# Kernel tuning notes

Hardware: AMD Instinct MI355X
Metric: run time of the kernel (lower is better)

The kernel has to match this reference:

```python
import jax, jax.numpy as jnp
import numpy as np

B, S, DIN, D, H, NL, DOUT = 1, 1024, 128, 512, 8, 4, 390
HD = D // H
MAXS = 1024  # max_seq_length; Er has 2*MAXS-1 rows
EPS = 1e-5


def _ln(x, g, b):
    m = jnp.mean(x, axis=-1, keepdims=True)
    v = jnp.mean((x - m) ** 2, axis=-1, keepdims=True)
    return (x - m) / jnp.sqrt(v + EPS) * g + b


def setup_inputs() -> dict:
    key = jax.random.key(0)
    ks = jax.random.split(key, 16)
    it = iter(ks)

    def w(shape, scale=0.02):
        return jax.random.normal(next(it), shape, jnp.float32) * scale

    return {
        "x": jax.random.normal(next(it), (B, S, DIN), jnp.float32),
        "emb_W": w((DIN, D)), "emb_b": jnp.zeros((D,), jnp.float32),
        "Wq": w((NL, D, D)), "bq": jnp.zeros((NL, D), jnp.float32),
        "Wk": w((NL, D, D)), "bk": jnp.zeros((NL, D), jnp.float32),
        "Wv": w((NL, D, D)), "bv": jnp.zeros((NL, D), jnp.float32),
        "Wo": w((NL, D, D)), "bo": jnp.zeros((NL, D), jnp.float32),
        "Er": w((NL, 2 * MAXS - 1, HD), 1.0),  # torch.randn init
        "ln1_g": jnp.ones((NL, D), jnp.float32), "ln1_b": jnp.zeros((NL, D), jnp.float32),
        "W1": w((NL, D, 4 * D)), "b1": jnp.zeros((NL, 4 * D), jnp.float32),
        "W2": w((NL, 4 * D, D)), "b2": jnp.zeros((NL, D), jnp.float32),
        "ln2_g": jnp.ones((NL, D), jnp.float32), "ln2_b": jnp.zeros((NL, D), jnp.float32),
        "lnf_g": jnp.ones((D,), jnp.float32), "lnf_b": jnp.zeros((D,), jnp.float32),
        "Wi": w((D, 2 * D)), "bi": jnp.zeros((2 * D,), jnp.float32),
        "Wf": w((2 * D, DOUT)), "bf": jnp.zeros((DOUT,), jnp.float32),
    }


def reference(x, emb_W, emb_b, Wq, bq, Wk, bk, Wv, bv, Wo, bo, Er,
              ln1_g, ln1_b, W1, b1, W2, b2, ln2_g, ln2_b,
              lnf_g, lnf_b, Wi, bi, Wf, bf):
    h = x @ emb_W + emb_b  # (B,S,D)
    # relative index table (S,S): (i - j) + S - 1, shared by all layers
    ri = (jnp.arange(S)[:, None] - jnp.arange(S)[None, :]) + (S - 1)
    scale = 1.0 / jnp.sqrt(jnp.float32(HD))
    for l in range(NL):
        res = h
        n = _ln(h, ln1_g[l], ln1_b[l])
        q = (n @ Wq[l] + bq[l]).reshape(B, S, H, HD).transpose(0, 2, 1, 3)  # (B,H,S,HD)
        k = (n @ Wk[l] + bk[l]).reshape(B, S, H, HD).transpose(0, 2, 1, 3)
        v = (n @ Wv[l] + bv[l]).reshape(B, S, H, HD).transpose(0, 2, 1, 3)
        scores = jnp.einsum('bhsd,bhtd->bhst', q, k) * scale  # (B,H,S,S)
        E = Er[l][ri]  # (S,S,HD) gathered relative embeddings
        rel = jnp.einsum('bhsd,std->bhst', q, E)  # note: NOT scaled (faithful)
        attn = jax.nn.softmax(scores + rel, axis=-1)  # no causal mask in source
        o = jnp.einsum('bhst,bhtd->bhsd', attn, v)
        o = o.transpose(0, 2, 1, 3).reshape(B, S, D)
        h = res + (o @ Wo[l] + bo[l])
        res = h
        n = _ln(h, ln2_g[l], ln2_b[l])
        f = jax.nn.gelu(n @ W1[l] + b1[l], approximate=False) @ W2[l] + b2[l]
        h = res + f
    h = _ln(h, lnf_g, lnf_b)
    h = jax.nn.gelu(h @ Wi + bi, approximate=False)
    return h @ Wf + bf  # (B,S,DOUT)
```

## Files before the change

### kernel.cpp

```cpp
#include <hip/hip_runtime.h>
#include <hip/hip_bf16.h>
#include <math.h>

#define SEQ 1024
#define DM 512
#define NH 8
#define HD 64
#define NLAYER 4
#define DIN 128
#define DFF 2048
#define DOUT 390
#define ERROWS 2047
#define NSPLIT 4

using u16 = unsigned short;
typedef __attribute__((ext_vector_type(8))) short short8;
typedef __attribute__((ext_vector_type(4))) float f32x4;

__device__ inline u16 f2bf(float f){
  __hip_bfloat16 h = __float2bfloat16(f);
  return *(u16*)&h;
}
__device__ inline float bf2f(u16 u){
  __hip_bfloat16 h; *(u16*)&h = u;
  return __bfloat162float(h);
}

__device__ inline float block_sum(float v, float* red){
  int tid = threadIdx.x;
  red[tid] = v; __syncthreads();
  for (int s = 128; s > 0; s >>= 1){
    if (tid < s) red[tid] += red[tid + s];
    __syncthreads();
  }
  float r = red[0]; __syncthreads();
  return r;
}

__global__ __launch_bounds__(256)
void prep_k(const float* __restrict__ x, const float* __restrict__ Er,
            const float* __restrict__ bq, const float* __restrict__ bk,
            const float* __restrict__ bv,
            const float* __restrict__ emb_W, const float* __restrict__ Wq,
            const float* __restrict__ Wk, const float* __restrict__ Wv,
            const float* __restrict__ Wo, const float* __restrict__ W1,
            const float* __restrict__ W2, const float* __restrict__ Wi,
            const float* __restrict__ Wf,
            u16* __restrict__ xb, u16* __restrict__ erB,
            float* __restrict__ qkvbias,
            u16* __restrict__ embT, u16* __restrict__ wqkvT,
            u16* __restrict__ woT, u16* __restrict__ w1T,
            u16* __restrict__ w2T, u16* __restrict__ wiT,
            u16* __restrict__ wfT)
{
  __shared__ float Ls[64][65];
  int b = blockIdx.x;
  const int tid = threadIdx.x;

  if (b < 128){
    int i = (b * 256 + tid) * 4;
    float4 v = *(const float4*)(x + i);
    xb[i+0]=f2bf(v.x); xb[i+1]=f2bf(v.y); xb[i+2]=f2bf(v.z); xb[i+3]=f2bf(v.w);
    return;
  }
  b -= 128;
  if (b < 512){
    int i = (b * 256 + tid) * 4;
    if (i < NLAYER * ERROWS * HD){
      float4 v = *(const float4*)(Er + i);
      erB[i+0]=f2bf(v.x); erB[i+1]=f2bf(v.y); erB[i+2]=f2bf(v.z); erB[i+3]=f2bf(v.w);
    }
    return;
  }
  b -= 512;
  if (b < 24){
    int i = b * 256 + tid;
    int l = i / 1536, c = i - l * 1536;
    float v = (c < 512) ? bq[l * 512 + c]
            : (c < 1024) ? bk[l * 512 + c - 512]
                         : bv[l * 512 + c - 1024];
    qkvbias[i] = v;
    return;
  }
  b -= 24;

  const float* W; u16* WT; int K, N, k0, n0;
  if (b < 16){
    W = emb_W; WT = embT; K = DIN; N = DM;
    k0 = (b & 1) * 64; n0 = (b >> 1) * 64;
  } else if (b < 1040){
    int i = b - 16, fam = i >> 8, w2 = i & 255, z = w2 >> 6, t2 = w2 & 63;
    K = DM; N = DM; k0 = (t2 & 7) * 64; n0 = (t2 >> 3) * 64;
    const float* Wsrc = (fam == 0) ? Wq : (fam == 1) ? Wk : (fam == 2) ? Wv : Wo;
    W = Wsrc + (long)z * DM * DM;
    WT = (fam < 3) ? wqkvT + (long)z * 1536 * DM + (long)fam * 512 * DM
                   : woT + (long)z * DM * DM;
  } else if (b < 2064){
    int i = b - 1040, z = i >> 8, w2 = i & 255;
    K = DM; N = DFF; k0 = (w2 & 7) * 64; n0 = (w2 >> 3) * 64;
    W = W1 + (long)z * DM * DFF; WT = w1T + (long)z * DFF * DM;
  } else if (b < 3088){
    int i = b - 2064, z = i >> 8, w2 = i & 255;
    K = DFF; N = DM; k0 = (w2 & 31) * 64; n0 = (w2 >> 5) * 64;
    W = W2 + (long)z * DFF * DM; WT = w2T + (long)z * DM * DFF;
  } else if (b < 3216){
    int i = b - 3088;
    K = DM; N = 2 * DM; k0 = (i & 7) * 64; n0 = (i >> 3) * 64;
    W = Wi; WT = wiT;
  } else {
    int i = b - 3216;
    K = 2 * DM; N = DOUT; k0 = (i & 15) * 64; n0 = (i >> 4) * 64;
    W = Wf; WT = wfT;
  }

  const int cr = (tid & 15) * 4, rr0 = tid >> 4;
#pragma unroll
  for (int rr = 0; rr < 4; rr++){
    int row = rr0 + rr * 16;
    const float* wp = W + (size_t)(k0 + row) * N + n0 + cr;
#pragma unroll
    for (int j = 0; j < 4; j++)
      Ls[row][cr + j] = (n0 + cr + j < N) ? wp[j] : 0.f;
  }
  __syncthreads();
  const int nrow = tid >> 2, kc = (tid & 3) * 16;
  const bool valid = (n0 + nrow) < N;
  u16 buf[16];
#pragma unroll
  for (int j = 0; j < 16; j++)
    buf[j] = valid ? f2bf(Ls[kc + j][nrow]) : (u16)0;
  u16* out = WT + (size_t)(n0 + nrow) * K + k0 + kc;
  ((uint4*)out)[0] = ((uint4*)buf)[0];
  ((uint4*)out)[1] = ((uint4*)buf)[1];
}

template<bool GELU, bool RES, bool BIAS, bool OUTBF>
__global__ __launch_bounds__(256)
void mgemm(const u16* __restrict__ A, const u16* __restrict__ B,
           const float* __restrict__ bias, const float* __restrict__ res,
           void* __restrict__ Cout, int N, int K,
           int lda, int ldb, int ldc)
{
  __shared__ u16 As[32][72];
  __shared__ u16 Bs[64][72];
  const int tid = threadIdx.x;
  const int row0 = blockIdx.y * 32, n0 = blockIdx.x * 64;
  const int w = tid >> 6, lane = tid & 63, m = lane & 15, quad = lane >> 4;
  const int rowg = w >> 1, colp = w & 1;
  const int ar = tid >> 3, akc = (tid & 7) * 8;
  const int br = tid >> 2, bkc = (tid & 3) * 16;

  f32x4 acc[2];
  acc[0] = (f32x4){0.f,0.f,0.f,0.f};
  acc[1] = (f32x4){0.f,0.f,0.f,0.f};

  uint4 pa  = *(const uint4*)&A[(long)(row0 + ar) * lda + akc];
  uint4 pb0 = *(const uint4*)&B[(long)(n0 + br) * ldb + bkc];
  uint4 pb1 = *(const uint4*)&B[(long)(n0 + br) * ldb + bkc + 8];

  for (int k0 = 0; k0 < K; k0 += 64){
    *(uint4*)&As[ar][akc]     = pa;
    *(uint4*)&Bs[br][bkc]     = pb0;
    *(uint4*)&Bs[br][bkc + 8] = pb1;
    __syncthreads();
    if (k0 + 64 < K){
      pa  = *(const uint4*)&A[(long)(row0 + ar) * lda + k0 + 64 + akc];
      pb0 = *(const uint4*)&B[(long)(n0 + br) * ldb + k0 + 64 + bkc];
      pb1 = *(const uint4*)&B[(long)(n0 + br) * ldb + k0 + 64 + bkc + 8];
    }
    short8 a0 = *(const short8*)&As[rowg * 16 + m][quad * 8];
    short8 a1 = *(const short8*)&As[rowg * 16 + m][32 + quad * 8];
#pragma unroll
    for (int c = 0; c < 2; c++){
      int colg = colp * 2 + c;
      short8 b0 = *(const short8*)&Bs[colg * 16 + m][quad * 8];
      short8 b1 = *(const short8*)&Bs[colg * 16 + m][32 + quad * 8];
      acc[c] = __builtin_amdgcn_mfma_f32_16x16x32_bf16(a0, b0, acc[c], 0, 0, 0);
      acc[c] = __builtin_amdgcn_mfma_f32_16x16x32_bf16(a1, b1, acc[c], 0, 0, 0);
    }
    __syncthreads();
  }

#pragma unroll
  for (int c = 0; c < 2; c++){
    int col = n0 + (colp * 2 + c) * 16 + m;
    if (col < N){
#pragma unroll
      for (int r = 0; r < 4; r++){
        int row = row0 + rowg * 16 + quad * 4 + r;
        float val = acc[c][r];
        if (BIAS) val += bias[col];
        if (RES)  val += res[(long)row * ldc + col];
        if (GELU) val = 0.5f * val * (1.f + erff(val * 0.70710678118f));
        if (OUTBF) ((u16*)Cout)[(long)row * ldc + col] = f2bf(val);
        else      ((float*)Cout)[(long)row * ldc + col] = val;
      }
    }
  }
}

__global__ __launch_bounds__(256)
void ln_k(const float* __restrict__ x, const float* __restrict__ g,
          const float* __restrict__ b, u16* __restrict__ out)
{
  __shared__ float red[256];
  const int r = blockIdx.x, tid = threadIdx.x;
  const float* xr = x + (size_t)r * DM;
  float v0 = xr[tid], v1 = xr[tid + 256];
  float mean = block_sum(v0 + v1, red) * (1.f / DM);
  float d0 = v0 - mean, d1 = v1 - mean;
  float var = block_sum(d0 * d0 + d1 * d1, red) * (1.f / DM);
  float inv = rsqrtf(var + 1e-5f);
  out[(size_t)r * DM + tid]       = f2bf(d0 * inv * g[tid]       + b[tid]);
  out[(size_t)r * DM + tid + 256] = f2bf(d1 * inv * g[tid + 256] + b[tid + 256]);
}

__global__ __launch_bounds__(256)
void flash_k(const u16* __restrict__ qkv, const u16* __restrict__ ErB,
             float* __restrict__ Op, float* __restrict__ ml)
{
  __shared__ u16 Qs[64][72];
  __shared__ u16 Ks[64][72];
  __shared__ u16 VsT[64][72];
  __shared__ u16 Es[128][72];
  __shared__ u16 Ts[64][136];
  __shared__ u16 Ps[64][72];

  const int tid = threadIdx.x;
  const int s0 = blockIdx.x * 64, hh = blockIdx.y, sp = blockIdx.z;
  const int w = tid >> 6, lane = tid & 63, m = lane & 15, quad = lane >> 4;

  {
    const int r = tid >> 2, kc = (tid & 3) * 16;
    const u16* qp = qkv + (size_t)(s0 + r) * 1536 + hh * HD + kc;
    *(uint4*)&Qs[r][kc]     = *(const uint4*)&qp[0];
    *(uint4*)&Qs[r][kc + 8] = *(const uint4*)&qp[8];
  }
  __syncthreads();

  const short8 a0 = *(const short8*)&Qs[w * 16 + m][quad * 8];
  const short8 a1 = *(const short8*)&Qs[w * 16 + m][32 + quad * 8];

  f32x4 accO[4];
#pragma unroll
  for (int c = 0; c < 4; c++) accO[c] = (f32x4){0.f, 0.f, 0.f, 0.f};
  float mrun[4], lrun[4];
#pragma unroll
  for (int r = 0; r < 4; r++){ mrun[r] = -1e30f; lrun[r] = 0.f; }

  const int tbeg = sp * (SEQ / NSPLIT), tend = tbeg + SEQ / NSPLIT;
  for (int t0 = tbeg; t0 < tend; t0 += 64){
    __syncthreads();
    {
      const int r = tid >> 2, kc = (tid & 3) * 16;
      const u16* kp = qkv + (size_t)(t0 + r) * 1536 + 512 + hh * HD + kc;
      *(uint4*)&Ks[r][kc]     = *(const uint4*)&kp[0];
      *(uint4*)&Ks[r][kc + 8] = *(const uint4*)&kp[8];
      const u16* vp = qkv + (size_t)(t0 + r) * 1536 + 1024 + hh * HD + kc;
      uint4 v0 = *(const uint4*)&vp[0];
      uint4 v1 = *(const uint4*)&vp[8];
      const u16* pv0 = (const u16*)&v0;
      const u16* pv1 = (const u16*)&v1;
#pragma unroll
      for (int j = 0; j < 8; j++) VsT[kc + j][r]     = pv0[j];
#pragma unroll
      for (int j = 0; j < 8; j++) VsT[kc + 8 + j][r] = pv1[j];
      const int rb = s0 - t0 + 960;
      for (int idx = tid; idx < 127 * 8; idx += 256){
        int er = idx >> 3, ekc = (idx & 7) * 8;
        *(uint4*)&Es[er][ekc] = *(const uint4*)&ErB[(size_t)(rb + er) * HD + ekc];
      }
      if (tid < 8){ uint4 z = {0,0,0,0}; *(uint4*)&Es[127][tid * 8] = z; }
    }
    __syncthreads();

    f32x4 qk[4], tt[8];
#pragma unroll
    for (int c = 0; c < 4; c++) qk[c] = (f32x4){0.f,0.f,0.f,0.f};
#pragma unroll
    for (int c = 0; c < 8; c++) tt[c] = (f32x4){0.f,0.f,0.f,0.f};
#pragma unroll
    for (int c = 0; c < 4; c++){
      short8 b0 = *(const short8*)&Ks[c * 16 + m][quad * 8];
      short8 b1 = *(const short8*)&Ks[c * 16 + m][32 + quad * 8];
      qk[c] = __builtin_amdgcn_mfma_f32_16x16x32_bf16(a0, b0, qk[c], 0, 0, 0);
      qk[c] = __builtin_amdgcn_mfma_f32_16x16x32_bf16(a1, b1, qk[c], 0, 0, 0);
    }
#pragma unroll
    for (int c = 0; c < 8; c++){
      short8 b0 = *(const short8*)&Es[c * 16 + m][quad * 8];
      short8 b1 = *(const short8*)&Es[c * 16 + m][32 + quad * 8];
      tt[c] = __builtin_amdgcn_mfma_f32_16x16x32_bf16(a0, b0, tt[c], 0, 0, 0);
      tt[c] = __builtin_amdgcn_mfma_f32_16x16x32_bf16(a1, b1, tt[c], 0, 0, 0);
    }
#pragma unroll
    for (int c = 0; c < 8; c++)
#pragma unroll
      for (int r = 0; r < 4; r++)
        Ts[w * 16 + quad * 4 + r][c * 16 + m] = f2bf(tt[c][r]);
    __syncthreads();

    float sv[4][4];
#pragma unroll
    for (int c = 0; c < 4; c++){
      int j = c * 16 + m;
#pragma unroll
      for (int r = 0; r < 4; r++){
        int i = w * 16 + quad * 4 + r;
        sv[c][r] = qk[c][r] * 0.125f + bf2f(Ts[i][i - j + 63]);
      }
    }
    float alpha[4];
#pragma unroll
    for (int r = 0; r < 4; r++){
      float rmax = fmaxf(fmaxf(sv[0][r], sv[1][r]), fmaxf(sv[2][r], sv[3][r]));
#pragma unroll
      for (int off = 1; off < 16; off <<= 1)
        rmax = fmaxf(rmax, __shfl_xor(rmax, off));
      float mnew = fmaxf(mrun[r], rmax);
      alpha[r] = __expf(mrun[r] - mnew);
      mrun[r] = mnew;
      float rsum = 0.f;
#pragma unroll
      for (int c = 0; c < 4; c++){
        float pv = __expf(sv[c][r] - mnew);
        sv[c][r] = pv;
        rsum += pv;
      }
#pragma unroll
      for (int off = 1; off < 16; off <<= 1)
        rsum += __shfl_xor(rsum, off);
      lrun[r] = lrun[r] * alpha[r] + rsum;
    }
#pragma unroll
    for (int c = 0; c < 4; c++)
#pragma unroll
      for (int r = 0; r < 4; r++)
        accO[c][r] *= alpha[r];
#pragma unroll
    for (int c = 0; c < 4; c++)
#pragma unroll
      for (int r = 0; r < 4; r++)
        Ps[w * 16 + quad * 4 + r][c * 16 + m] = f2bf(sv[c][r]);
    __syncthreads();

    short8 pa0 = *(const short8*)&Ps[w * 16 + m][quad * 8];
    short8 pa1 = *(const short8*)&Ps[w * 16 + m][32 + quad * 8];
#pragma unroll
    for (int c = 0; c < 4; c++){
      short8 b0 = *(const short8*)&VsT[c * 16 + m][quad * 8];
      short8 b1 = *(const short8*)&VsT[c * 16 + m][32 + quad * 8];
      accO[c] = __builtin_amdgcn_mfma_f32_16x16x32_bf16(pa0, b0, accO[c], 0, 0, 0);
      accO[c] = __builtin_amdgcn_mfma_f32_16x16x32_bf16(pa1, b1, accO[c], 0, 0, 0);
    }
  }

  const long base = ((long)sp * NH + hh) * SEQ;
#pragma unroll
  for (int c = 0; c < 4; c++){
#pragma unroll
    for (int r = 0; r < 4; r++){
      int row = s0 + w * 16 + quad * 4 + r;
      Op[(base + row) * HD + c * 16 + m] = accO[c][r];
    }
  }
  if (m == 0){
#pragma unroll
    for (int r = 0; r < 4; r++){
      int row = s0 + w * 16 + quad * 4 + r;
      ml[(base + row) * 2 + 0] = mrun[r];
      ml[(base + row) * 2 + 1] = lrun[r];
    }
  }
}

__global__ __launch_bounds__(256)
void fcomb_k(const float* __restrict__ Op, const float* __restrict__ ml,
             u16* __restrict__ o)
{
  const int s = blockIdx.x, tid = threadIdx.x;
  const int hh = tid >> 5, c0 = (tid & 31) * 2;
  float mm[NSPLIT], ll[NSPLIT];
#pragma unroll
  for (int sp = 0; sp < NSPLIT; sp++){
    long b = (((long)sp * NH + hh) * SEQ + s) * 2;
    mm[sp] = ml[b]; ll[sp] = ml[b + 1];
  }
  float ms = fmaxf(fmaxf(mm[0], mm[1]), fmaxf(mm[2], mm[3]));
  float o0 = 0.f, o1 = 0.f, lsum = 0.f;
#pragma unroll
  for (int sp = 0; sp < NSPLIT; sp++){
    float wsp = __expf(mm[sp] - ms);
    lsum += wsp * ll[sp];
    const float* op = Op + (((long)sp * NH + hh) * SEQ + s) * HD + c0;
    o0 += wsp * op[0];
    o1 += wsp * op[1];
  }
  float inv = 1.f / lsum;
  o[(size_t)s * DM + hh * HD + c0]     = f2bf(o0 * inv);
  o[(size_t)s * DM + hh * HD + c0 + 1] = f2bf(o1 * inv);
}

extern "C" void kernel_launch(void* const* d_in, const int* in_sizes, int n_in,
                              void* d_out, int out_size, void* d_ws, size_t ws_size,
                              hipStream_t stream) {
  const float* x     = (const float*)d_in[0];
  const float* emb_W = (const float*)d_in[1];
  const float* emb_b = (const float*)d_in[2];
  const float* Wq    = (const float*)d_in[3];
  const float* bq    = (const float*)d_in[4];
  const float* Wk    = (const float*)d_in[5];
  const float* bk    = (const float*)d_in[6];
  const float* Wv    = (const float*)d_in[7];
  const float* bv    = (const float*)d_in[8];
  const float* Wo    = (const float*)d_in[9];
  const float* bo    = (const float*)d_in[10];
  const float* Er    = (const float*)d_in[11];
  const float* ln1_g = (const float*)d_in[12];
  const float* ln1_b = (const float*)d_in[13];
  const float* W1    = (const float*)d_in[14];
  const float* b1    = (const float*)d_in[15];
  const float* W2    = (const float*)d_in[16];
  const float* b2    = (const float*)d_in[17];
  const float* ln2_g = (const float*)d_in[18];
  const float* ln2_b = (const float*)d_in[19];
  const float* lnf_g = (const float*)d_in[20];
  const float* lnf_b = (const float*)d_in[21];
  const float* Wi    = (const float*)d_in[22];
  const float* bi    = (const float*)d_in[23];
  const float* Wf    = (const float*)d_in[24];
  const float* bfin  = (const float*)d_in[25];

  u16* p = (u16*)d_ws;
  u16* xb    = p; p += SEQ * DIN;
  u16* embT  = p; p += DM * DIN;
  u16* wqkvT = p; p += (size_t)NLAYER * 1536 * DM;
  u16* woT   = p; p += (size_t)NLAYER * DM * DM;
  u16* w1T   = p; p += (size_t)NLAYER * DFF * DM;
  u16* w2T   = p; p += (size_t)NLAYER * DM * DFF;
  u16* wiT   = p; p += (size_t)(2 * DM) * DM;
  u16* wfT   = p; p += (size_t)448 * (2 * DM);
  u16* erB   = p; p += (size_t)NLAYER * ERROWS * HD;
  u16* nb    = p; p += SEQ * DM;
  u16* qkvb  = p; p += (size_t)SEQ * 1536;
  u16* ob    = p; p += SEQ * DM;
  u16* mid   = p; p += (size_t)SEQ * DFF;
  float* qkvbias = (float*)p;
  float* hb  = qkvbias + NLAYER * 1536;
  float* Op  = hb + SEQ * DM;
  float* mlb = Op + (size_t)NSPLIT * NH * SEQ * HD;

  dim3 blk(256);

  prep_k<<<3992, blk, 0, stream>>>(
      x, Er, bq, bk, bv, emb_W, Wq, Wk, Wv, Wo, W1, W2, Wi, Wf,
      xb, erB, qkvbias, embT, wqkvT, woT, w1T, w2T, wiT, wfT);

  dim3 g512(8, 32), gqkv(24, 32), gff(32, 32), gwi(16, 32), gout(7, 32);
  dim3 gfl(16, NH, NSPLIT);

  mgemm<false, false, true, false><<<g512, blk, 0, stream>>>(
      xb, embT, emb_b, nullptr, hb, DM, DIN, DIN, DIN, DM);

  for (int l = 0; l < NLAYER; l++) {
    const u16* wqkvT_l = wqkvT + (size_t)l * 1536 * DM;
    const u16* woT_l   = woT + (size_t)l * DM * DM;
    const u16* w1T_l   = w1T + (size_t)l * DFF * DM;
    const u16* w2T_l   = w2T + (size_t)l * DM * DFF;
    const u16* erB_l   = erB + (size_t)l * ERROWS * HD;

    ln_k<<<SEQ, blk, 0, stream>>>(hb, ln1_g + l * DM, ln1_b + l * DM, nb);
    mgemm<false, false, true, true><<<gqkv, blk, 0, stream>>>(
        nb, wqkvT_l, qkvbias + l * 1536, nullptr, qkvb, 1536, DM, DM, DM, 1536);

    flash_k<<<gfl, blk, 0, stream>>>(qkvb, erB_l, Op, mlb);
    fcomb_k<<<SEQ, blk, 0, stream>>>(Op, mlb, ob);

    mgemm<false, true, true, false><<<g512, blk, 0, stream>>>(
        ob, woT_l, bo + l * DM, hb, hb, DM, DM, DM, DM, DM);

    ln_k<<<SEQ, blk, 0, stream>>>(hb, ln2_g + l * DM, ln2_b + l * DM, nb);
    mgemm<true, false, true, true><<<gff, blk, 0, stream>>>(
        nb, w1T_l, b1 + l * DFF, nullptr, mid, DFF, DM, DM, DM, DFF);
    mgemm<false, true, true, false><<<g512, blk, 0, stream>>>(
        mid, w2T_l, b2 + l * DM, hb, hb, DM, DFF, DFF, DFF, DM);
  }

  ln_k<<<SEQ, blk, 0, stream>>>(hb, lnf_g, lnf_b, nb);
  mgemm<true, false, true, true><<<gwi, blk, 0, stream>>>(
      nb, wiT, bi, nullptr, mid, 2 * DM, DM, DM, DM, 2 * DM);
  mgemm<false, false, true, false><<<gout, blk, 0, stream>>>(
      mid, wfT, bfin, nullptr, (float*)d_out, DOUT, 2 * DM, 2 * DM, 2 * DM, DOUT);
}
```

Baseline: 457.5 us.

## Use direct global-to-LDS loads with XOR swizzle in GEMM; warp-per-row layernorm

```diff
diff --git a/kernel.cpp b/kernel.cpp
--- a/kernel.cpp
+++ b/kernel.cpp
@@ -17,6 +17,13 @@
 typedef __attribute__((ext_vector_type(8))) short short8;
 typedef __attribute__((ext_vector_type(4))) float f32x4;
 
+typedef __attribute__((address_space(1))) const u16 gas_u16;
+typedef __attribute__((address_space(3))) u16 las_u16;
+
+__device__ inline void gload_lds16(const u16* g, u16* l){
+  __builtin_amdgcn_global_load_lds((gas_u16*)g, (las_u16*)l, 16, 0, 0);
+}
+
 __device__ inline u16 f2bf(float f){
   __hip_bfloat16 h = __float2bfloat16(f);
   return *(u16*)&h;
@@ -24,17 +31,6 @@
 __device__ inline float bf2f(u16 u){
   __hip_bfloat16 h; *(u16*)&h = u;
   return __bfloat162float(h);
-}
-
-__device__ inline float block_sum(float v, float* red){
-  int tid = threadIdx.x;
-  red[tid] = v; __syncthreads();
-  for (int s = 128; s > 0; s >>= 1){
-    if (tid < s) red[tid] += red[tid + s];
-    __syncthreads();
-  }
-  float r = red[0]; __syncthreads();
-  return r;
 }
 
 __global__ __launch_bounds__(256)
@@ -141,40 +137,40 @@
            void* __restrict__ Cout, int N, int K,
            int lda, int ldb, int ldc)
 {
-  __shared__ u16 As[32][72];
-  __shared__ u16 Bs[64][72];
+  __shared__ u16 As[32][64];
+  __shared__ u16 Bs[64][64];
   const int tid = threadIdx.x;
   const int row0 = blockIdx.y * 32, n0 = blockIdx.x * 64;
   const int w = tid >> 6, lane = tid & 63, m = lane & 15, quad = lane >> 4;
   const int rowg = w >> 1, colp = w & 1;
-  const int ar = tid >> 3, akc = (tid & 7) * 8;
-  const int br = tid >> 2, bkc = (tid & 3) * 16;
+
+  const int arr  = w * 8 + (lane >> 3);
+  const int acg  = ((lane & 7) ^ (arr & 7)) * 8;
+  const int brr0 = w * 16 + (lane >> 3);
+  const int brr1 = brr0 + 8;
+  const int bcg0 = ((lane & 7) ^ (brr0 & 7)) * 8;
+  const int bcg1 = ((lane & 7) ^ (brr1 & 7)) * 8;
+
+  const int sw  = m & 7;
+  const int cS0 = ((quad ^ sw) << 3);
+  const int cS1 = (((quad + 4) ^ sw) << 3);
 
   f32x4 acc[2];
   acc[0] = (f32x4){0.f,0.f,0.f,0.f};
   acc[1] = (f32x4){0.f,0.f,0.f,0.f};
 
-  uint4 pa  = *(const uint4*)&A[(long)(row0 + ar) * lda + akc];
-  uint4 pb0 = *(const uint4*)&B[(long)(n0 + br) * ldb + bkc];
-  uint4 pb1 = *(const uint4*)&B[(long)(n0 + br) * ldb + bkc + 8];
-
   for (int k0 = 0; k0 < K; k0 += 64){
-    *(uint4*)&As[ar][akc]     = pa;
-    *(uint4*)&Bs[br][bkc]     = pb0;
-    *(uint4*)&Bs[br][bkc + 8] = pb1;
+    gload_lds16(A + (long)(row0 + arr)  * lda + k0 + acg,  &As[w * 8][0]);
+    gload_lds16(B + (long)(n0 + brr0) * ldb + k0 + bcg0, &Bs[w * 16][0]);
+    gload_lds16(B + (long)(n0 + brr1) * ldb + k0 + bcg1, &Bs[w * 16 + 8][0]);
     __syncthreads();
-    if (k0 + 64 < K){
-      pa  = *(const uint4*)&A[(long)(row0 + ar) * lda + k0 + 64 + akc];
-      pb0 = *(const uint4*)&B[(long)(n0 + br) * ldb + k0 + 64 + bkc];
-      pb1 = *(const uint4*)&B[(long)(n0 + br) * ldb + k0 + 64 + bkc + 8];
-    }
-    short8 a0 = *(const short8*)&As[rowg * 16 + m][quad * 8];
-    short8 a1 = *(const short8*)&As[rowg * 16 + m][32 + quad * 8];
+    short8 a0 = *(const short8*)&As[rowg * 16 + m][cS0];
+    short8 a1 = *(const short8*)&As[rowg * 16 + m][cS1];
 #pragma unroll
     for (int c = 0; c < 2; c++){
       int colg = colp * 2 + c;
-      short8 b0 = *(const short8*)&Bs[colg * 16 + m][quad * 8];
-      short8 b1 = *(const short8*)&Bs[colg * 16 + m][32 + quad * 8];
+      short8 b0 = *(const short8*)&Bs[colg * 16 + m][cS0];
+      short8 b1 = *(const short8*)&Bs[colg * 16 + m][cS1];
       acc[c] = __builtin_amdgcn_mfma_f32_16x16x32_bf16(a0, b0, acc[c], 0, 0, 0);
       acc[c] = __builtin_amdgcn_mfma_f32_16x16x32_bf16(a1, b1, acc[c], 0, 0, 0);
     }
@@ -203,16 +199,33 @@
 void ln_k(const float* __restrict__ x, const float* __restrict__ g,
           const float* __restrict__ b, u16* __restrict__ out)
 {
-  __shared__ float red[256];
-  const int r = blockIdx.x, tid = threadIdx.x;
-  const float* xr = x + (size_t)r * DM;
-  float v0 = xr[tid], v1 = xr[tid + 256];
-  float mean = block_sum(v0 + v1, red) * (1.f / DM);
-  float d0 = v0 - mean, d1 = v1 - mean;
-  float var = block_sum(d0 * d0 + d1 * d1, red) * (1.f / DM);
-  float inv = rsqrtf(var + 1e-5f);
-  out[(size_t)r * DM + tid]       = f2bf(d0 * inv * g[tid]       + b[tid]);
-  out[(size_t)r * DM + tid + 256] = f2bf(d1 * inv * g[tid + 256] + b[tid + 256]);
+  const int w = threadIdx.x >> 6, lane = threadIdx.x & 63;
+  const int r = blockIdx.x * 4 + w;
+  const float4* xr = (const float4*)(x + (long)r * DM + lane * 8);
+  float4 v0 = xr[0], v1 = xr[1];
+  float s = v0.x+v0.y+v0.z+v0.w + v1.x+v1.y+v1.z+v1.w;
+  float q = v0.x*v0.x+v0.y*v0.y+v0.z*v0.z+v0.w*v0.w
+          + v1.x*v1.x+v1.y*v1.y+v1.z*v1.z+v1.w*v1.w;
+#pragma unroll
+  for (int off = 1; off < 64; off <<= 1){
+    s += __shfl_xor(s, off);
+    q += __shfl_xor(q, off);
+  }
+  float mn = s * (1.f / DM);
+  float inv = rsqrtf(q * (1.f / DM) - mn * mn + 1e-5f);
+  const float4* gp = (const float4*)(g + lane * 8);
+  const float4* bp = (const float4*)(b + lane * 8);
+  float4 g0 = gp[0], g1 = gp[1], b0 = bp[0], b1 = bp[1];
+  u16 tmp[8];
+  tmp[0] = f2bf((v0.x - mn) * inv * g0.x + b0.x);
+  tmp[1] = f2bf((v0.y - mn) * inv * g0.y + b0.y);
+  tmp[2] = f2bf((v0.z - mn) * inv * g0.z + b0.z);
+  tmp[3] = f2bf((v0.w - mn) * inv * g0.w + b0.w);
+  tmp[4] = f2bf((v1.x - mn) * inv * g1.x + b1.x);
+  tmp[5] = f2bf((v1.y - mn) * inv * g1.y + b1.y);
+  tmp[6] = f2bf((v1.z - mn) * inv * g1.z + b1.z);
+  tmp[7] = f2bf((v1.w - mn) * inv * g1.w + b1.w);
+  *(uint4*)(out + (long)r * DM + lane * 8) = *(uint4*)tmp;
 }
 
 __global__ __launch_bounds__(256)
@@ -458,6 +471,7 @@
 
   dim3 g512(8, 32), gqkv(24, 32), gff(32, 32), gwi(16, 32), gout(7, 32);
   dim3 gfl(16, NH, NSPLIT);
+  dim3 gln(SEQ / 4);
 
   mgemm<false, false, true, false><<<g512, blk, 0, stream>>>(
       xb, embT, emb_b, nullptr, hb, DM, DIN, DIN, DIN, DM);
@@ -469,7 +483,7 @@
     const u16* w2T_l   = w2T + (size_t)l * DM * DFF;
     const u16* erB_l   = erB + (size_t)l * ERROWS * HD;
 
-    ln_k<<<SEQ, blk, 0, stream>>>(hb, ln1_g + l * DM, ln1_b + l * DM, nb);
+    ln_k<<<gln, blk, 0, stream>>>(hb, ln1_g + l * DM, ln1_b + l * DM, nb);
     mgemm<false, false, true, true><<<gqkv, blk, 0, stream>>>(
         nb, wqkvT_l, qkvbias + l * 1536, nullptr, qkvb, 1536, DM, DM, DM, 1536);
 
@@ -479,14 +493,14 @@
     mgemm<false, true, true, false><<<g512, blk, 0, stream>>>(
         ob, woT_l, bo + l * DM, hb, hb, DM, DM, DM, DM, DM);
 
-    ln_k<<<SEQ, blk, 0, stream>>>(hb, ln2_g + l * DM, ln2_b + l * DM, nb);
+    ln_k<<<gln, blk, 0, stream>>>(hb, ln2_g + l * DM, ln2_b + l * DM, nb);
     mgemm<true, false, true, true><<<gff, blk, 0, stream>>>(
         nb, w1T_l, b1 + l * DFF, nullptr, mid, DFF, DM, DM, DM, DFF);
     mgemm<false, true, true, false><<<g512, blk, 0, stream>>>(
         mid, w2T_l, b2 + l * DM, hb, hb, DM, DFF, DFF, DFF, DM);
   }
 
-  ln_k<<<SEQ, blk, 0, stream>>>(hb, lnf_g, lnf_b, nb);
+  ln_k<<<gln, blk, 0, stream>>>(hb, lnf_g, lnf_b, nb);
   mgemm<true, false, true, true><<<gwi, blk, 0, stream>>>(
       nb, wiT, bi, nullptr, mid, 2 * DM, DM, DM, DM, 2 * DM);
   mgemm<false, false, true, false><<<gout, blk, 0, stream>>>(
```

After: 458.3 us. About the same (+0.2%).

## Fuse LayerNorm into following GEMMs and split-combine into Wo GEMM

Applied to the files above, without the earlier changes.

```diff
diff --git a/kernel.cpp b/kernel.cpp
--- a/kernel.cpp
+++ b/kernel.cpp
@@ -24,17 +24,6 @@
 __device__ inline float bf2f(u16 u){
   __hip_bfloat16 h; *(u16*)&h = u;
   return __bfloat162float(h);
-}
-
-__device__ inline float block_sum(float v, float* red){
-  int tid = threadIdx.x;
-  red[tid] = v; __syncthreads();
-  for (int s = 128; s > 0; s >>= 1){
-    if (tid < s) red[tid] += red[tid + s];
-    __syncthreads();
-  }
-  float r = red[0]; __syncthreads();
-  return r;
 }
 
 __global__ __launch_bounds__(256)
@@ -199,20 +188,194 @@
   }
 }
 
+template<bool GELU>
 __global__ __launch_bounds__(256)
-void ln_k(const float* __restrict__ x, const float* __restrict__ g,
-          const float* __restrict__ b, u16* __restrict__ out)
+void mgemm_ln(const float* __restrict__ Afp, const float* __restrict__ lng,
+              const float* __restrict__ lnb, const u16* __restrict__ B,
+              const float* __restrict__ bias, u16* __restrict__ Cout,
+              int N, int ldc)
 {
-  __shared__ float red[256];
-  const int r = blockIdx.x, tid = threadIdx.x;
-  const float* xr = x + (size_t)r * DM;
-  float v0 = xr[tid], v1 = xr[tid + 256];
-  float mean = block_sum(v0 + v1, red) * (1.f / DM);
-  float d0 = v0 - mean, d1 = v1 - mean;
-  float var = block_sum(d0 * d0 + d1 * d1, red) * (1.f / DM);
-  float inv = rsqrtf(var + 1e-5f);
-  out[(size_t)r * DM + tid]       = f2bf(d0 * inv * g[tid]       + b[tid]);
-  out[(size_t)r * DM + tid + 256] = f2bf(d1 * inv * g[tid + 256] + b[tid + 256]);
+  __shared__ u16 As[32][520];
+  __shared__ u16 Bs[64][72];
+  const int tid = threadIdx.x;
+  const int row0 = blockIdx.y * 32, n0 = blockIdx.x * 64;
+
+  {
+    const int r = tid >> 3, cl = tid & 7;
+    const float* xr = Afp + (long)(row0 + r) * 512;
+    float4 va[8], vb[8];
+    float s = 0.f, q = 0.f;
+#pragma unroll
+    for (int jj = 0; jj < 8; jj++){
+      int c0 = cl * 8 + 64 * jj;
+      va[jj] = *(const float4*)(xr + c0);
+      vb[jj] = *(const float4*)(xr + c0 + 4);
+      s += va[jj].x + va[jj].y + va[jj].z + va[jj].w
+         + vb[jj].x + vb[jj].y + vb[jj].z + vb[jj].w;
+      q += va[jj].x*va[jj].x + va[jj].y*va[jj].y + va[jj].z*va[jj].z + va[jj].w*va[jj].w
+         + vb[jj].x*vb[jj].x + vb[jj].y*vb[jj].y + vb[jj].z*vb[jj].z + vb[jj].w*vb[jj].w;
+    }
+#pragma unroll
+    for (int off = 1; off < 8; off <<= 1){
+      s += __shfl_xor(s, off);
+      q += __shfl_xor(q, off);
+    }
+    float mn = s * (1.f / 512.f);
+    float inv = rsqrtf(q * (1.f / 512.f) - mn * mn + 1e-5f);
+#pragma unroll
+    for (int jj = 0; jj < 8; jj++){
+      int c0 = cl * 8 + 64 * jj;
+      float4 g0 = *(const float4*)(lng + c0), g1 = *(const float4*)(lng + c0 + 4);
+      float4 b0 = *(const float4*)(lnb + c0), b1 = *(const float4*)(lnb + c0 + 4);
+      u16 t2[8];
+      t2[0] = f2bf((va[jj].x - mn) * inv * g0.x + b0.x);
+      t2[1] = f2bf((va[jj].y - mn) * inv * g0.y + b0.y);
+      t2[2] = f2bf((va[jj].z - mn) * inv * g0.z + b0.z);
+      t2[3] = f2bf((va[jj].w - mn) * inv * g0.w + b0.w);
+      t2[4] = f2bf((vb[jj].x - mn) * inv * g1.x + b1.x);
+      t2[5] = f2bf((vb[jj].y - mn) * inv * g1.y + b1.y);
+      t2[6] = f2bf((vb[jj].z - mn) * inv * g1.z + b1.z);
+      t2[7] = f2bf((vb[jj].w - mn) * inv * g1.w + b1.w);
+      *(uint4*)&As[r][c0] = *(uint4*)t2;
+    }
+  }
+
+  const int w = tid >> 6, lane = tid & 63, m = lane & 15, quad = lane >> 4;
+  const int rowg = w >> 1, colp = w & 1;
+  const int br = tid >> 2, bkc = (tid & 3) * 16;
+
+  f32x4 acc[2];
+  acc[0] = (f32x4){0.f,0.f,0.f,0.f};
+  acc[1] = (f32x4){0.f,0.f,0.f,0.f};
+
+  uint4 pb0 = *(const uint4*)&B[(long)(n0 + br) * 512 + bkc];
+  uint4 pb1 = *(const uint4*)&B[(long)(n0 + br) * 512 + bkc + 8];
+
+  for (int k0 = 0; k0 < 512; k0 += 64){
+    *(uint4*)&Bs[br][bkc]     = pb0;
+    *(uint4*)&Bs[br][bkc + 8] = pb1;
+    __syncthreads();
+    if (k0 + 64 < 512){
+      pb0 = *(const uint4*)&B[(long)(n0 + br) * 512 + k0 + 64 + bkc];
+      pb1 = *(const uint4*)&B[(long)(n0 + br) * 512 + k0 + 64 + bkc + 8];
+    }
+    short8 a0 = *(const short8*)&As[rowg * 16 + m][k0 + quad * 8];
+    short8 a1 = *(const short8*)&As[rowg * 16 + m][k0 + 32 + quad * 8];
+#pragma unroll
+    for (int c = 0; c < 2; c++){
+      int colg = colp * 2 + c;
+      short8 b0 = *(const short8*)&Bs[colg * 16 + m][quad * 8];
+      short8 b1 = *(const short8*)&Bs[colg * 16 + m][32 + quad * 8];
+      acc[c] = __builtin_amdgcn_mfma_f32_16x16x32_bf16(a0, b0, acc[c], 0, 0, 0);
+      acc[c] = __builtin_amdgcn_mfma_f32_16x16x32_bf16(a1, b1, acc[c], 0, 0, 0);
+    }
+    __syncthreads();
+  }
+
+#pragma unroll
+  for (int c = 0; c < 2; c++){
+    int col = n0 + (colp * 2 + c) * 16 + m;
+#pragma unroll
+    for (int r = 0; r < 4; r++){
+      int row = row0 + rowg * 16 + quad * 4 + r;
+      float val = acc[c][r] + bias[col];
+      if (GELU) val = 0.5f * val * (1.f + erff(val * 0.70710678118f));
+      Cout[(long)row * ldc + col] = f2bf(val);
+    }
+  }
+}
+
+__global__ __launch_bounds__(256)
+void wo_comb(const float* __restrict__ Op, const float* __restrict__ ml,
+             const u16* __restrict__ B, const float* __restrict__ bias,
+             float* __restrict__ hb)
+{
+  __shared__ u16 As[32][520];
+  __shared__ u16 Bs[64][72];
+  const int tid = threadIdx.x;
+  const int row0 = blockIdx.y * 32, n0 = blockIdx.x * 64;
+
+  {
+    const int r = tid >> 3, cl = tid & 7;
+    const int s = row0 + r;
+#pragma unroll
+    for (int jj = 0; jj < 8; jj++){
+      float mm[NSPLIT], ll[NSPLIT];
+#pragma unroll
+      for (int sp = 0; sp < NSPLIT; sp++){
+        long bix = (((long)sp * NH + jj) * SEQ + s) * 2;
+        mm[sp] = ml[bix]; ll[sp] = ml[bix + 1];
+      }
+      float ms = fmaxf(fmaxf(mm[0], mm[1]), fmaxf(mm[2], mm[3]));
+      float wsp[NSPLIT], lsum = 0.f;
+#pragma unroll
+      for (int sp = 0; sp < NSPLIT; sp++){
+        wsp[sp] = __expf(mm[sp] - ms);
+        lsum += wsp[sp] * ll[sp];
+      }
+      float winv = 1.f / lsum;
+      float o[8];
+#pragma unroll
+      for (int j = 0; j < 8; j++) o[j] = 0.f;
+#pragma unroll
+      for (int sp = 0; sp < NSPLIT; sp++){
+        const float* op = Op + (((long)sp * NH + jj) * SEQ + s) * HD + cl * 8;
+        float4 u0 = *(const float4*)(op);
+        float4 u1 = *(const float4*)(op + 4);
+        o[0] += wsp[sp] * u0.x; o[1] += wsp[sp] * u0.y;
+        o[2] += wsp[sp] * u0.z; o[3] += wsp[sp] * u0.w;
+        o[4] += wsp[sp] * u1.x; o[5] += wsp[sp] * u1.y;
+        o[6] += wsp[sp] * u1.z; o[7] += wsp[sp] * u1.w;
+      }
+      u16 t2[8];
+#pragma unroll
+      for (int j = 0; j < 8; j++) t2[j] = f2bf(o[j] * winv);
+      *(uint4*)&As[r][cl * 8 + 64 * jj] = *(uint4*)t2;
+    }
+  }
+
+  const int w = tid >> 6, lane = tid & 63, m = lane & 15, quad = lane >> 4;
+  const int rowg = w >> 1, colp = w & 1;
+  const int br = tid >> 2, bkc = (tid & 3) * 16;
+
+  f32x4 acc[2];
+  acc[0] = (f32x4){0.f,0.f,0.f,0.f};
+  acc[1] = (f32x4){0.f,0.f,0.f,0.f};
+
+  uint4 pb0 = *(const uint4*)&B[(long)(n0 + br) * 512 + bkc];
+  uint4 pb1 = *(const uint4*)&B[(long)(n0 + br) * 512 + bkc + 8];
+
+  for (int k0 = 0; k0 < 512; k0 += 64){
+    *(uint4*)&Bs[br][bkc]     = pb0;
+    *(uint4*)&Bs[br][bkc + 8] = pb1;
+    __syncthreads();
+    if (k0 + 64 < 512){
+      pb0 = *(const uint4*)&B[(long)(n0 + br) * 512 + k0 + 64 + bkc];
+      pb1 = *(const uint4*)&B[(long)(n0 + br) * 512 + k0 + 64 + bkc + 8];
+    }
+    short8 a0 = *(const short8*)&As[rowg * 16 + m][k0 + quad * 8];
+    short8 a1 = *(const short8*)&As[rowg * 16 + m][k0 + 32 + quad * 8];
+#pragma unroll
+    for (int c = 0; c < 2; c++){
+      int colg = colp * 2 + c;
+      short8 b0 = *(const short8*)&Bs[colg * 16 + m][quad * 8];
+      short8 b1 = *(const short8*)&Bs[colg * 16 + m][32 + quad * 8];
+      acc[c] = __builtin_amdgcn_mfma_f32_16x16x32_bf16(a0, b0, acc[c], 0, 0, 0);
+      acc[c] = __builtin_amdgcn_mfma_f32_16x16x32_bf16(a1, b1, acc[c], 0, 0, 0);
+    }
+    __syncthreads();
+  }
+
+#pragma unroll
+  for (int c = 0; c < 2; c++){
+    int col = n0 + (colp * 2 + c) * 16 + m;
+#pragma unroll
+    for (int r = 0; r < 4; r++){
+      int row = row0 + rowg * 16 + quad * 4 + r;
+      float val = acc[c][r] + bias[col] + hb[(long)row * DM + col];
+      hb[(long)row * DM + col] = val;
+    }
+  }
 }
 
 __global__ __launch_bounds__(256)
@@ -372,33 +535,6 @@
       ml[(base + row) * 2 + 1] = lrun[r];
     }
   }
-}
-
-__global__ __launch_bounds__(256)
-void fcomb_k(const float* __restrict__ Op, const float* __restrict__ ml,
-             u16* __restrict__ o)
-{
-  const int s = blockIdx.x, tid = threadIdx.x;
-  const int hh = tid >> 5, c0 = (tid & 31) * 2;
-  float mm[NSPLIT], ll[NSPLIT];
-#pragma unroll
-  for (int sp = 0; sp < NSPLIT; sp++){
-    long b = (((long)sp * NH + hh) * SEQ + s) * 2;
-    mm[sp] = ml[b]; ll[sp] = ml[b + 1];
-  }
-  float ms = fmaxf(fmaxf(mm[0], mm[1]), fmaxf(mm[2], mm[3]));
-  float o0 = 0.f, o1 = 0.f, lsum = 0.f;
-#pragma unroll
-  for (int sp = 0; sp < NSPLIT; sp++){
-    float wsp = __expf(mm[sp] - ms);
-    lsum += wsp * ll[sp];
-    const float* op = Op + (((long)sp * NH + hh) * SEQ + s) * HD + c0;
-    o0 += wsp * op[0];
-    o1 += wsp * op[1];
-  }
-  float inv = 1.f / lsum;
-  o[(size_t)s * DM + hh * HD + c0]     = f2bf(o0 * inv);
-  o[(size_t)s * DM + hh * HD + c0 + 1] = f2bf(o1 * inv);
 }
 
 extern "C" void kernel_launch(void* const* d_in, const int* in_sizes, int n_in,
@@ -441,9 +577,7 @@
   u16* wiT   = p; p += (size_t)(2 * DM) * DM;
   u16* wfT   = p; p += (size_t)448 * (2 * DM);
   u16* erB   = p; p += (size_t)NLAYER * ERROWS * HD;
-  u16* nb    = p; p += SEQ * DM;
   u16* qkvb  = p; p += (size_t)SEQ * 1536;
-  u16* ob    = p; p += SEQ * DM;
   u16* mid   = p; p += (size_t)SEQ * DFF;
   float* qkvbias = (float*)p;
   float* hb  = qkvbias + NLAYER * 1536;
@@ -469,26 +603,24 @@
     const u16* w2T_l   = w2T + (size_t)l * DM * DFF;
     const u16* erB_l   = erB + (size_t)l * ERROWS * HD;
 
-    ln_k<<<SEQ, blk, 0, stream>>>(hb, ln1_g + l * DM, ln1_b + l * DM, nb);
-    mgemm<false, false, true, true><<<gqkv, blk, 0, stream>>>(
-        nb, wqkvT_l, qkvbias + l * 1536, nullptr, qkvb, 1536, DM, DM, DM, 1536);
+    mgemm_ln<false><<<gqkv, blk, 0, stream>>>(
+        hb, ln1_g + l * DM, ln1_b + l * DM, wqkvT_l, qkvbias + l * 1536,
+        qkvb, 1536, 1536);
 
     flash_k<<<gfl, blk, 0, stream>>>(qkvb, erB_l, Op, mlb);
-    fcomb_k<<<SEQ, blk, 0, stream>>>(Op, mlb, ob);
-
-    mgemm<false, true, true, false><<<g512, blk, 0, stream>>>(
-        ob, woT_l, bo + l * DM, hb, hb, DM, DM, DM, DM, DM);
-
-    ln_k<<<SEQ, blk, 0, stream>>>(hb, ln2_g + l * DM, ln2_b + l * DM, nb);
-    mgemm<true, false, true, true><<<gff, blk, 0, stream>>>(
-        nb, w1T_l, b1 + l * DFF, nullptr, mid, DFF, DM, DM, DM, DFF);
+
+    wo_comb<<<g512, blk, 0, stream>>>(Op, mlb, woT_l, bo + l * DM, hb);
+
+    mgemm_ln<true><<<gff, blk, 0, stream>>>(
+        hb, ln2_g + l * DM, ln2_b + l * DM, w1T_l, b1 + l * DFF,
+        mid, DFF, DFF);
+
     mgemm<false, true, true, false><<<g512, blk, 0, stream>>>(
         mid, w2T_l, b2 + l * DM, hb, hb, DM, DFF, DFF, DFF, DM);
   }
 
-  ln_k<<<SEQ, blk, 0, stream>>>(hb, lnf_g, lnf_b, nb);
-  mgemm<true, false, true, true><<<gwi, blk, 0, stream>>>(
-      nb, wiT, bi, nullptr, mid, 2 * DM, DM, DM, DM, 2 * DM);
+  mgemm_ln<true><<<gwi, blk, 0, stream>>>(
+      hb, lnf_g, lnf_b, wiT, bi, mid, 2 * DM, 2 * DM);
   mgemm<false, false, true, false><<<gout, blk, 0, stream>>>(
       mid, wfT, bfin, nullptr, (float*)d_out, DOUT, 2 * DM, 2 * DM, 2 * DM, DOUT);
 }
```

After: 474.0 us. 3.6% more time.
